# Kernel tuning notes

Measured on AMD Instinct MI355X. Metric: run time of the kernel, lower is better.

Reference implementation:

```python
import jax, jax.numpy as jnp
import numpy as np

KERNEL = 3
STRIDE = 1
PADDING = 1


def setup_inputs() -> dict:
    key = jax.random.key(0)
    k1, k2, k3 = jax.random.split(key, 3)
    x = jax.random.normal(k1, (8, 64, 128, 128), dtype=jnp.float32)
    # AdderLayer weight [O, C, kH, kW] and bias [O]
    w = jax.random.normal(k2, (64, 64, KERNEL, KERNEL), dtype=jnp.float32) * 0.1
    b = jax.random.normal(k3, (64,), dtype=jnp.float32)
    return {"x": x, "w": w, "b": b}


def _adder_conv_relu(x, w, b):
    # AdderNet conv: out[n,o,h,w] = -sum_{c,kh,kw} |x_patch - w[o]| (+ bias), then ReLU.
    N, C, H, W = x.shape
    O = w.shape[0]
    k = w.shape[2]
    # Extract patches: [N, C*k*k, Ho, Wo] (C is the slowest-varying feature dim,
    # matching w.reshape(O, -1) ordering)
    patches = jax.lax.conv_general_dilated_patches(
        x, (k, k), (STRIDE, STRIDE), [(PADDING, PADDING), (PADDING, PADDING)])
    Ho, Wo = patches.shape[2], patches.shape[3]
    P = patches.transpose(0, 2, 3, 1).reshape(-1, C * k * k)  # [N*Ho*Wo, Ckk]
    wf = w.reshape(O, -1)  # [O, Ckk]

    @jax.checkpoint
    def per_out(wb):
        wrow, bi = wb  # [Ckk], scalar
        # negative L1 distance + bias, fused with ReLU
        return jax.nn.relu(bi - jnp.abs(P - wrow[None, :]).sum(-1))  # [N*Ho*Wo]

    out = jax.lax.map(per_out, (wf, b))  # [O, N*Ho*Wo]
    return out.reshape(O, N, Ho, Wo).transpose(1, 0, 2, 3)  # [N, O, Ho, Wo]


def reference(x, w, b):
    return _adder_conv_relu(x, w, b)
```

## Files before the change

### kernel.cpp

```cpp
#include <hip/hip_runtime.h>

typedef unsigned int u32;


#define Hh 128
#define Ww 128
#define C_IN 64
#define O_OUT 64
#define NB 8
#define PIX (Hh * Ww)

__global__ __launch_bounds__(256)
void adder_row_screen(const float* __restrict__ x, const float* __restrict__ w,
                      const float* __restrict__ b, float* __restrict__ out) {
    __shared__ float Ap[8 * 128];
    __shared__ float Afin[128];
    __shared__ float wmax[4];
    __shared__ u32   nfail;
    __shared__ u32   flist[128];

    const int tid = threadIdx.x;
    const int bid = blockIdx.x;
    const int n   = bid >> 7;
    const int h   = bid & 127;

    if (tid == 0) nfail = 0;

    const int c4 = tid & 31;
    const int g  = tid >> 5;
    const float4* xn = (const float4*)x + (size_t)n * C_IN * (PIX / 4)
                     + (size_t)h * (Ww / 4) + c4;
    const float4 a0 = xn[(size_t)g * (PIX / 4)];
    const float4 a1 = xn[(size_t)(g + 8) * (PIX / 4)];

    {
        const int o = tid >> 2, jj = tid & 3;
        float s = 0.f;
        #pragma unroll
        for (int k = 0; k < 4; ++k) {
            const float* wp = w + (size_t)o * 576 + (jj * 4 + k) * 9 + 3;
            s += fabsf(wp[0]) + fabsf(wp[1]) + fabsf(wp[2]);
        }
        s += __shfl_xor(s, 1); s += __shfl_xor(s, 2);
        float v = s + b[o];
        #pragma unroll
        for (int d = 4; d < 64; d <<= 1) v = fmaxf(v, __shfl_xor(v, d));
        if ((tid & 63) == 0) wmax[tid >> 6] = v;
    }

    {
        float4 a;
        a.x = fabsf(a0.x) + fabsf(a1.x); a.y = fabsf(a0.y) + fabsf(a1.y);
        a.z = fabsf(a0.z) + fabsf(a1.z); a.w = fabsf(a0.w) + fabsf(a1.w);
        *(float4*)&Ap[g * 128 + c4 * 4] = a;
    }
    __syncthreads();

    if (tid < 128) {
        float s = 0.f;
        #pragma unroll
        for (int gg = 0; gg < 8; ++gg) s += Ap[gg * 128 + tid];
        Afin[tid] = s;
    }
    __syncthreads();

    const float thr = fmaxf(fmaxf(wmax[0], wmax[1]),
                            fmaxf(wmax[2], wmax[3])) + 1.0f;

    if (tid < 128) {
        float S = Afin[tid];
        if (tid > 0)   S += Afin[tid - 1];
        if (tid < 127) S += Afin[tid + 1];
        if (!(S >= thr)) {
            u32 k = atomicAdd(&nfail, 1u);
            flist[k] = (u32)tid;
        }
    }
    __syncthreads();
    const u32 nf = nfail;

    float4* outn = (float4*)out + (size_t)n * O_OUT * (PIX / 4);
    const float4 z = make_float4(0.f, 0.f, 0.f, 0.f);
    #pragma unroll
    for (int j = 0; j < 8; ++j) {
        const int idx = (j << 8) + tid;
        const int o = idx >> 5, cc = idx & 31;
        outn[(size_t)o * (PIX / 4) + h * (Ww / 4) + cc] = z;
    }

    if (nf) {
        __syncthreads();
        const float* xs = x + (size_t)n * C_IN * PIX;
        for (u32 i = tid; i < nf * 64u; i += 256u) {
            const int col = (int)flist[i >> 6];
            const int o   = (int)(i & 63u);
            const float* wo = w + (size_t)o * C_IN * 9;
            float sum = 0.f;
            for (int c = 0; c < C_IN; ++c) {
                const float* xc = xs + (size_t)c * PIX;
                const float* wc = wo + c * 9;
                #pragma unroll
                for (int kh = 0; kh < 3; ++kh) {
                    const int gh = h + kh - 1;
                    #pragma unroll
                    for (int kw = 0; kw < 3; ++kw) {
                        const int gw = col + kw - 1;
                        const float xval = ((unsigned)gh < (unsigned)Hh &&
                                            (unsigned)gw < (unsigned)Ww)
                                           ? xc[gh * Ww + gw] : 0.f;
                        sum += fabsf(xval - wc[kh * 3 + kw]);
                    }
                }
            }
            out[(size_t)(n * O_OUT + o) * PIX + h * Ww + col] = fmaxf(b[o] - sum, 0.f);
        }
    }
}

extern "C" void kernel_launch(void* const* d_in, const int* in_sizes, int n_in,
                              void* d_out, int out_size, void* d_ws, size_t ws_size,
                              hipStream_t stream) {
    const float* x = (const float*)d_in[0];
    const float* w = (const float*)d_in[1];
    const float* b = (const float*)d_in[2];
    float* out = (float*)d_out;

    adder_row_screen<<<NB * Hh, 256, 0, stream>>>(x, w, b, out);
}
```

Before: 12.98 us.

## Screen four-row tiles per 1024-thread block with ballot fail masks

Each block now handles four consecutive output rows with 1024 threads instead of one row with 256. The zero-fill stores therefore become 2KB contiguous runs per output channel, and block count and per-block setup (weight bound reduction, syncs) are amortised. The atomic-counter fail list is replaced with wave ballots into 64-bit masks. The exact fallback now assigns one failing pixel per wave, round-robin, with lanes mapping to output channels. The cost is only 256 blocks with large blocks, which may reduce latency hiding and leave some CUs unevenly loaded.

```diff
diff --git a/kernel.cpp b/kernel.cpp
--- a/kernel.cpp
+++ b/kernel.cpp
@@ -1,6 +1,7 @@
 #include <hip/hip_runtime.h>
 
 typedef unsigned int u32;
+typedef unsigned long long u64;
 
 
 #define Hh 128
@@ -9,110 +10,126 @@
 #define O_OUT 64
 #define NB 8
 #define PIX (Hh * Ww)
+#define RT 4
+#define APD 516
 
-__global__ __launch_bounds__(256)
-void adder_row_screen(const float* __restrict__ x, const float* __restrict__ w,
-                      const float* __restrict__ b, float* __restrict__ out) {
-    __shared__ float Ap[8 * 128];
-    __shared__ float Afin[128];
-    __shared__ float wmax[4];
-    __shared__ u32   nfail;
-    __shared__ u32   flist[128];
+__global__ __launch_bounds__(1024)
+void adder_tile_screen(const float* __restrict__ x, const float* __restrict__ w,
+                       const float* __restrict__ b, float* __restrict__ out) {
+    __shared__ float ApF[8 * APD];
+    __shared__ float Afin[512];
+    __shared__ float wmax[16];
+    __shared__ u64   fmask[8];
 
-    const int tid = threadIdx.x;
-    const int bid = blockIdx.x;
-    const int n   = bid >> 7;
-    const int h   = bid & 127;
+    const int tid  = threadIdx.x;
+    const int bid  = blockIdx.x;
+    const int n    = bid >> 5;
+    const int h0   = (bid & 31) * RT;
+    const int wid  = tid >> 6;
+    const int lane = tid & 63;
 
-    if (tid == 0) nfail = 0;
-
-    const int c4 = tid & 31;
-    const int g  = tid >> 5;
-    const float4* xn = (const float4*)x + (size_t)n * C_IN * (PIX / 4)
-                     + (size_t)h * (Ww / 4) + c4;
-    const float4 a0 = xn[(size_t)g * (PIX / 4)];
-    const float4 a1 = xn[(size_t)(g + 8) * (PIX / 4)];
+    const int g    = tid >> 7;
+    const int pos  = tid & 127;
+    const int prow = pos >> 5, pc4 = pos & 31;
+    const float4* xp = (const float4*)x + (size_t)n * C_IN * (PIX / 4)
+                     + (size_t)(h0 + prow) * (Ww / 4) + pc4;
+    const float4 va = xp[(size_t)g * (PIX / 4)];
+    const float4 vb = xp[(size_t)(g + 8) * (PIX / 4)];
 
     {
-        const int o = tid >> 2, jj = tid & 3;
-        float s = 0.f;
-        #pragma unroll
-        for (int k = 0; k < 4; ++k) {
-            const float* wp = w + (size_t)o * 576 + (jj * 4 + k) * 9 + 3;
-            s += fabsf(wp[0]) + fabsf(wp[1]) + fabsf(wp[2]);
-        }
+        const int o = tid >> 4, jj = tid & 15;
+        const float* wp = w + (size_t)o * 576 + jj * 9 + 3;
+        float s = fabsf(wp[0]) + fabsf(wp[1]) + fabsf(wp[2]);
         s += __shfl_xor(s, 1); s += __shfl_xor(s, 2);
+        s += __shfl_xor(s, 4); s += __shfl_xor(s, 8);
         float v = s + b[o];
-        #pragma unroll
-        for (int d = 4; d < 64; d <<= 1) v = fmaxf(v, __shfl_xor(v, d));
-        if ((tid & 63) == 0) wmax[tid >> 6] = v;
+        v = fmaxf(v, __shfl_xor(v, 16));
+        v = fmaxf(v, __shfl_xor(v, 32));
+        if (lane == 0) wmax[wid] = v;
     }
 
     {
         float4 a;
-        a.x = fabsf(a0.x) + fabsf(a1.x); a.y = fabsf(a0.y) + fabsf(a1.y);
-        a.z = fabsf(a0.z) + fabsf(a1.z); a.w = fabsf(a0.w) + fabsf(a1.w);
-        *(float4*)&Ap[g * 128 + c4 * 4] = a;
+        a.x = fabsf(va.x) + fabsf(vb.x); a.y = fabsf(va.y) + fabsf(vb.y);
+        a.z = fabsf(va.z) + fabsf(vb.z); a.w = fabsf(va.w) + fabsf(vb.w);
+        *(float4*)&ApF[g * APD + pos * 4] = a;
     }
     __syncthreads();
 
-    if (tid < 128) {
+    float thr = wmax[0];
+    #pragma unroll
+    for (int i = 1; i < 16; ++i) thr = fmaxf(thr, wmax[i]);
+    thr += 1.0f;
+
+    if (tid < 512) {
         float s = 0.f;
         #pragma unroll
-        for (int gg = 0; gg < 8; ++gg) s += Ap[gg * 128 + tid];
+        for (int gg = 0; gg < 8; ++gg) s += ApF[gg * APD + tid];
         Afin[tid] = s;
     }
     __syncthreads();
 
-    const float thr = fmaxf(fmaxf(wmax[0], wmax[1]),
-                            fmaxf(wmax[2], wmax[3])) + 1.0f;
-
-    if (tid < 128) {
+    if (tid < 512) {
+        const int col = tid & 127;
         float S = Afin[tid];
-        if (tid > 0)   S += Afin[tid - 1];
-        if (tid < 127) S += Afin[tid + 1];
-        if (!(S >= thr)) {
-            u32 k = atomicAdd(&nfail, 1u);
-            flist[k] = (u32)tid;
-        }
+        if (col > 0)   S += Afin[tid - 1];
+        if (col < 127) S += Afin[tid + 1];
+        const bool fail = !(S >= thr);
+        const u64 bal = __ballot(fail);
+        if (lane == 0) fmask[wid] = bal;
     }
     __syncthreads();
-    const u32 nf = nfail;
+
+    u64 any = fmask[0];
+    #pragma unroll
+    for (int v = 1; v < 8; ++v) any |= fmask[v];
 
     float4* outn = (float4*)out + (size_t)n * O_OUT * (PIX / 4);
     const float4 z = make_float4(0.f, 0.f, 0.f, 0.f);
     #pragma unroll
-    for (int j = 0; j < 8; ++j) {
-        const int idx = (j << 8) + tid;
-        const int o = idx >> 5, cc = idx & 31;
-        outn[(size_t)o * (PIX / 4) + h * (Ww / 4) + cc] = z;
+    for (int oo = 0; oo < 4; ++oo) {
+        float4* dst = outn + (size_t)(wid * 4 + oo) * (PIX / 4) + h0 * (Ww / 4);
+        dst[lane]      = z;
+        dst[lane + 64] = z;
     }
 
-    if (nf) {
+    if (any) {
         __syncthreads();
         const float* xs = x + (size_t)n * C_IN * PIX;
-        for (u32 i = tid; i < nf * 64u; i += 256u) {
-            const int col = (int)flist[i >> 6];
-            const int o   = (int)(i & 63u);
-            const float* wo = w + (size_t)o * C_IN * 9;
-            float sum = 0.f;
-            for (int c = 0; c < C_IN; ++c) {
-                const float* xc = xs + (size_t)c * PIX;
-                const float* wc = wo + c * 9;
-                #pragma unroll
-                for (int kh = 0; kh < 3; ++kh) {
-                    const int gh = h + kh - 1;
-                    #pragma unroll
-                    for (int kw = 0; kw < 3; ++kw) {
-                        const int gw = col + kw - 1;
-                        const float xval = ((unsigned)gh < (unsigned)Hh &&
-                                            (unsigned)gw < (unsigned)Ww)
-                                           ? xc[gh * Ww + gw] : 0.f;
-                        sum += fabsf(xval - wc[kh * 3 + kw]);
+        int k = 0;
+        for (int v = 0; v < 8; ++v) {
+            u64 m = fmask[v];
+            while (m) {
+                const int bit = __ffsll((unsigned long long)m) - 1;
+                m &= m - 1;
+                if ((k & 15) == wid) {
+                    const int p   = v * 64 + bit;
+                    const int row = p >> 7, col = p & 127;
+                    const int h   = h0 + row;
+                    const int o   = lane;
+                    const float* wo = w + (size_t)o * C_IN * 9;
+                    float sum = 0.f;
+                    for (int c = 0; c < C_IN; ++c) {
+                        const float* xc = xs + (size_t)c * PIX;
+                        const float* wc = wo + c * 9;
+                        #pragma unroll
+                        for (int kh = 0; kh < 3; ++kh) {
+                            const int gh = h + kh - 1;
+                            #pragma unroll
+                            for (int kw = 0; kw < 3; ++kw) {
+                                const int gw = col + kw - 1;
+                                const float xval = ((unsigned)gh < (unsigned)Hh &&
+                                                    (unsigned)gw < (unsigned)Ww)
+                                                   ? xc[gh * Ww + gw] : 0.f;
+                                sum += fabsf(xval - wc[kh * 3 + kw]);
+                            }
+                        }
                     }
+                    out[(size_t)(n * O_OUT + o) * PIX + h * Ww + col] =
+                        fmaxf(b[o] - sum, 0.f);
                 }
+                ++k;
             }
-            out[(size_t)(n * O_OUT + o) * PIX + h * Ww + col] = fmaxf(b[o] - sum, 0.f);
         }
     }
 }
@@ -125,5 +142,5 @@
     const float* b = (const float*)d_in[2];
     float* out = (float*)d_out;
 
-    adder_row_screen<<<NB * Hh, 256, 0, stream>>>(x, w, b, out);
+    adder_tile_screen<<<NB * (Hh / RT), 1024, 0, stream>>>(x, w, b, out);
 }
```

New measurement: 14.83 us. 14.3% more time.
